# Optimization experiments

Measured on AMD Instinct MI355X. Metric: run time of the kernel, lower is better.

## Reference

```python
import jax, jax.numpy as jnp
import numpy as np

B, IN, H, OUT = 1_000_000, 64, 128, 2


def setup_inputs() -> dict:
    key = jax.random.key(0)
    k1, k2, k3, k4 = jax.random.split(key, 4)
    x = jax.random.normal(k1, (B, IN), dtype=jnp.float32)
    u = jax.random.randint(k2, (B,), 0, 3, dtype=jnp.int64)
    # Xavier-uniform-ish init for weights, zeros for biases (as in the module)
    lim1 = float(np.sqrt(6.0 / (IN + H)))
    W1 = jax.random.uniform(k3, (H, IN), dtype=jnp.float32, minval=-lim1, maxval=lim1)
    b1 = jnp.zeros((H,), dtype=jnp.float32)
    lim2 = float(np.sqrt(6.0 / (H + OUT)))
    Wb = jax.random.uniform(k4, (3, OUT, H), dtype=jnp.float32, minval=-lim2, maxval=lim2)
    bb = jnp.zeros((3, OUT), dtype=jnp.float32)
    return {"x": x, "u": u, "W1": W1, "b1": b1, "Wb": Wb, "bb": bb}


def reference(x, u, W1, b1, Wb, bb):
    # shared trunk: linear + relu  -> [B, H]
    h = jax.nn.relu(x @ W1.T + b1)
    # compute all 3 branch heads in one batched GEMM -> [B, 3, OUT]
    out_all = jnp.einsum("bh,koh->bko", h, Wb) + bb
    # hard routing: select head k = u[b] per row (equivalent to gather->scatter)
    u_idx = u.reshape(-1).astype(jnp.int32)
    out = jnp.take_along_axis(out_all, u_idx[:, None, None], axis=1)[:, 0, :]
    return out
```

## Files before the change

### kernel.cpp

```cpp
#include <hip/hip_runtime.h>
#include <stdint.h>


typedef float f32x4 __attribute__((ext_vector_type(4)));
typedef int   i32x4 __attribute__((ext_vector_type(4)));
typedef short short8 __attribute__((ext_vector_type(8)));
typedef __bf16 bf16x8 __attribute__((ext_vector_type(8)));

#define GLOBAL_AS __attribute__((address_space(1)))
#define LDS_AS    __attribute__((address_space(3)))

static __device__ __forceinline__ f32x4 mfma16(bf16x8 a, bf16x8 b, f32x4 c) {
    return __builtin_amdgcn_mfma_f32_16x16x32_bf16(a, b, c, 0, 0, 0);
}

__global__ __launch_bounds__(256) void coil_fused(
    const float* __restrict__ x,
    const int*   __restrict__ u,
    const float* __restrict__ W1,
    const float* __restrict__ b1,
    const float* __restrict__ Wb,
    const float* __restrict__ bb,
    float* __restrict__ out,
    int nPairs, int nWaves)
{
    __shared__ short w1s[128 * 64];
    __shared__ float b1s[128];
    __shared__ float xsl[4][2048];

    const int tid  = threadIdx.x;
    const int lane = tid & 63;
    const int c    = lane & 15;
    const int g    = lane >> 4;
    const int wsl  = tid >> 6;

    for (int qq = tid; qq < 1024; qq += 256) {
        int row = qq >> 3;
        const float* src = W1 + row * 64 + (qq & 7) * 8;
        short8 v;
        #pragma unroll
        for (int j = 0; j < 8; ++j) v[j] = __builtin_bit_cast(short, (__bf16)src[j]);
        int phys = (qq * 16) ^ ((row & 7) << 4);
        *reinterpret_cast<short8*>(reinterpret_cast<char*>(w1s) + phys) = v;
    }
    if (tid < 128) b1s[tid] = b1[tid];

    const int ko = c;
    const bool kvalid = (ko < 6);
    bf16x8 B2[4];
    #pragma unroll
    for (int s = 0; s < 4; ++s) {
        #pragma unroll
        for (int j = 0; j < 8; ++j) {
            int n = 32 * s + ((j >> 2) << 4) + 4 * g + (j & 3);
            B2[s][j] = kvalid ? (__bf16)Wb[ko * 128 + n] : (__bf16)0.0f;
        }
    }
    const float bbr = kvalid ? bb[ko] : 0.0f;
    const int khead = ko >> 1, opos = ko & 1;

    __syncthreads();

    int xoff[8];
    #pragma unroll
    for (int i = 0; i < 8; ++i) {
        int p = i * 1024 + lane * 16;
        xoff[i] = p ^ (((p >> 8) & 7) << 4);
    }

    const int sw  = (c & 7) << 4;
    const int r00 = (c * 256 + g * 32 +   0) ^ sw;
    const int r01 = (c * 256 + g * 32 +  16) ^ sw;
    const int r10 = (c * 256 + g * 32 + 128) ^ sw;
    const int r11 = (c * 256 + g * 32 + 144) ^ sw;

    const char* xb8 = reinterpret_cast<const char*>(x);
    const char* w1b = reinterpret_cast<const char*>(w1s);
    float* slot = &xsl[wsl][0];
    LDS_AS char* dst = (LDS_AS char*)slot;
    const char* sb = reinterpret_cast<const char*>(slot);

    auto stage = [&](int pairIdx, i32x4& uvA, i32x4& uvB) {
        const int t0 = pairIdx * 2;
        uvA = *reinterpret_cast<const i32x4*>(u + t0 * 16 + 4 * g);
        uvB = *reinterpret_cast<const i32x4*>(u + t0 * 16 + 16 + 4 * g);
        const char* src = xb8 + (size_t)t0 * 4096;
        #pragma unroll
        for (int i = 0; i < 8; ++i)
            __builtin_amdgcn_global_load_lds((const GLOBAL_AS void*)(src + xoff[i]),
                                             (LDS_AS void*)(dst + i * 1024), 16, 0, 0);
    };

    const int w = blockIdx.x * 4 + wsl;
    const int qv = nPairs / nWaves, rm = nPairs % nWaves;
    int p          = w * qv + (w < rm ? w : rm);
    const int pend = p + qv + (w < rm ? 1 : 0);
    if (p >= pend) return;

    i32x4 uvA, uvB, nuvA, nuvB;
    stage(p, uvA, uvB);

    for (; p < pend; ++p) {
        f32x4 xaA = *reinterpret_cast<const f32x4*>(sb + r00);
        f32x4 xbA = *reinterpret_cast<const f32x4*>(sb + r01);
        f32x4 xcA = *reinterpret_cast<const f32x4*>(sb + r10);
        f32x4 xdA = *reinterpret_cast<const f32x4*>(sb + r11);
        f32x4 xaB = *reinterpret_cast<const f32x4*>(sb + 4096 + r00);
        f32x4 xbB = *reinterpret_cast<const f32x4*>(sb + 4096 + r01);
        f32x4 xcB = *reinterpret_cast<const f32x4*>(sb + 4096 + r10);
        f32x4 xdB = *reinterpret_cast<const f32x4*>(sb + 4096 + r11);

        asm volatile("s_waitcnt lgkmcnt(0)" ::: "memory");

        stage((p + 1 < pend) ? p + 1 : p, nuvA, nuvB);

        bf16x8 B1aA, B1bA, B1aB, B1bB;
        #pragma unroll
        for (int j = 0; j < 4; ++j) {
            B1aA[j] = (__bf16)xaA[j];  B1aA[4 + j] = (__bf16)xbA[j];
            B1bA[j] = (__bf16)xcA[j];  B1bA[4 + j] = (__bf16)xdA[j];
            B1aB[j] = (__bf16)xaB[j];  B1aB[4 + j] = (__bf16)xbB[j];
            B1bB[j] = (__bf16)xcB[j];  B1bB[4 + j] = (__bf16)xdB[j];
        }

        f32x4 oaccA = {0.f, 0.f, 0.f, 0.f};
        f32x4 oaccB = {0.f, 0.f, 0.f, 0.f};
        #pragma unroll
        for (int s = 0; s < 4; ++s) {
            const int t0 = 2 * s, t1 = 2 * s + 1;
            f32x4 bia0 = *reinterpret_cast<const f32x4*>(&b1s[16 * t0 + 4 * g]);
            f32x4 bia1 = *reinterpret_cast<const f32x4*>(&b1s[16 * t1 + 4 * g]);
            const int lo0 = (16 * t0 + c) * 128 + 16 * g;
            const int lo1 = (16 * t1 + c) * 128 + 16 * g;
            short8 A00 = *reinterpret_cast<const short8*>(w1b + (lo0 ^ sw));
            short8 A01 = *reinterpret_cast<const short8*>(w1b + ((lo0 + 64) ^ sw));
            short8 A10 = *reinterpret_cast<const short8*>(w1b + (lo1 ^ sw));
            short8 A11 = *reinterpret_cast<const short8*>(w1b + ((lo1 + 64) ^ sw));
            f32x4 h0A = bia0, h1A = bia1, h0B = bia0, h1B = bia1;
            h0A = mfma16(__builtin_bit_cast(bf16x8, A00), B1aA, h0A);
            h0B = mfma16(__builtin_bit_cast(bf16x8, A00), B1aB, h0B);
            h1A = mfma16(__builtin_bit_cast(bf16x8, A10), B1aA, h1A);
            h1B = mfma16(__builtin_bit_cast(bf16x8, A10), B1aB, h1B);
            h0A = mfma16(__builtin_bit_cast(bf16x8, A01), B1bA, h0A);
            h0B = mfma16(__builtin_bit_cast(bf16x8, A01), B1bB, h0B);
            h1A = mfma16(__builtin_bit_cast(bf16x8, A11), B1bA, h1A);
            h1B = mfma16(__builtin_bit_cast(bf16x8, A11), B1bB, h1B);
            bf16x8 A2A, A2B;
            #pragma unroll
            for (int j = 0; j < 4; ++j) {
                A2A[j]     = (__bf16)fmaxf(h0A[j], 0.0f);
                A2A[4 + j] = (__bf16)fmaxf(h1A[j], 0.0f);
                A2B[j]     = (__bf16)fmaxf(h0B[j], 0.0f);
                A2B[4 + j] = (__bf16)fmaxf(h1B[j], 0.0f);
            }
            oaccA = mfma16(A2A, B2[s], oaccA);
            oaccB = mfma16(A2B, B2[s], oaccB);
        }

        const int m0 = p * 32 + 4 * g;
        if (khead == uvA[0]) out[(m0 +  0) * 2 + opos] = oaccA[0] + bbr;
        if (khead == uvA[1]) out[(m0 +  1) * 2 + opos] = oaccA[1] + bbr;
        if (khead == uvA[2]) out[(m0 +  2) * 2 + opos] = oaccA[2] + bbr;
        if (khead == uvA[3]) out[(m0 +  3) * 2 + opos] = oaccA[3] + bbr;
        if (khead == uvB[0]) out[(m0 + 16) * 2 + opos] = oaccB[0] + bbr;
        if (khead == uvB[1]) out[(m0 + 17) * 2 + opos] = oaccB[1] + bbr;
        if (khead == uvB[2]) out[(m0 + 18) * 2 + opos] = oaccB[2] + bbr;
        if (khead == uvB[3]) out[(m0 + 19) * 2 + opos] = oaccB[3] + bbr;

        uvA = nuvA; uvB = nuvB;
    }
}

extern "C" void kernel_launch(void* const* d_in, const int* in_sizes, int n_in,
                              void* d_out, int out_size, void* d_ws, size_t ws_size,
                              hipStream_t stream) {
    const float* x  = (const float*)d_in[0];
    const int*   u  = (const int*)d_in[1];
    const float* W1 = (const float*)d_in[2];
    const float* b1 = (const float*)d_in[3];
    const float* Wb = (const float*)d_in[4];
    const float* bb = (const float*)d_in[5];
    float* out = (float*)d_out;

    const int B = in_sizes[1];
    const int nTiles = B / 16;
    const int nPairs = nTiles / 2;

    int blocks = 768;
    int nWaves = blocks * 4;
    if (nWaves > nPairs) { blocks = (nPairs + 3) / 4; nWaves = blocks * 4; }

    hipLaunchKernelGGL(coil_fused, dim3(blocks), dim3(256), 0, stream,
                       x, u, W1, b1, Wb, bb, out, nPairs, nWaves);
}
```

Measured before the change: 53.17 us.

## Hold W1 fragments in registers and shrink blocks to two waves

The W1 tile is no longer staged into LDS; each lane now loads its bf16 A-fragments straight into 16 register vectors, which removes the per-iteration LDS reads of W1. Blocks shrink to 128 threads with 1536 blocks, and the prologue is reordered so the first x prefetch is issued before the W1 load. The MFMA chains for the two row tiles are serialised to limit live accumulators. In exchange, register pressure per wave rises (64 extra VGPRs for W1) and may lower occupancy, while less LDS is needed per block.

```diff
diff --git a/kernel.cpp b/kernel.cpp
--- a/kernel.cpp
+++ b/kernel.cpp
@@ -14,7 +14,7 @@
     return __builtin_amdgcn_mfma_f32_16x16x32_bf16(a, b, c, 0, 0, 0);
 }
 
-__global__ __launch_bounds__(256) void coil_fused(
+__global__ __launch_bounds__(128) void coil_fused(
     const float* __restrict__ x,
     const int*   __restrict__ u,
     const float* __restrict__ W1,
@@ -24,9 +24,8 @@
     float* __restrict__ out,
     int nPairs, int nWaves)
 {
-    __shared__ short w1s[128 * 64];
     __shared__ float b1s[128];
-    __shared__ float xsl[4][2048];
+    __shared__ float xsl[2][2048];
 
     const int tid  = threadIdx.x;
     const int lane = tid & 63;
@@ -34,16 +33,55 @@
     const int g    = lane >> 4;
     const int wsl  = tid >> 6;
 
-    for (int qq = tid; qq < 1024; qq += 256) {
-        int row = qq >> 3;
-        const float* src = W1 + row * 64 + (qq & 7) * 8;
-        short8 v;
-        #pragma unroll
-        for (int j = 0; j < 8; ++j) v[j] = __builtin_bit_cast(short, (__bf16)src[j]);
-        int phys = (qq * 16) ^ ((row & 7) << 4);
-        *reinterpret_cast<short8*>(reinterpret_cast<char*>(w1s) + phys) = v;
-    }
-    if (tid < 128) b1s[tid] = b1[tid];
+    int xoff[8];
+    #pragma unroll
+    for (int i = 0; i < 8; ++i) {
+        int pb = i * 1024 + lane * 16;
+        xoff[i] = pb ^ (((pb >> 8) & 7) << 4);
+    }
+
+    const char* xb8 = reinterpret_cast<const char*>(x);
+    float* slot = &xsl[wsl][0];
+    LDS_AS char* dst = (LDS_AS char*)slot;
+    const char* sb = reinterpret_cast<const char*>(slot);
+
+    auto stage = [&](int pairIdx, i32x4& uvA, i32x4& uvB) {
+        const int t0 = pairIdx * 2;
+        uvA = *reinterpret_cast<const i32x4*>(u + t0 * 16 + 4 * g);
+        uvB = *reinterpret_cast<const i32x4*>(u + t0 * 16 + 16 + 4 * g);
+        const char* src = xb8 + (size_t)t0 * 4096;
+        #pragma unroll
+        for (int i = 0; i < 8; ++i)
+            __builtin_amdgcn_global_load_lds((const GLOBAL_AS void*)(src + xoff[i]),
+                                             (LDS_AS void*)(dst + i * 1024), 16, 0, 0);
+    };
+
+    const int w = blockIdx.x * 2 + wsl;
+    const int qv = nPairs / nWaves, rm = nPairs % nWaves;
+    int p          = w * qv + (w < rm ? w : rm);
+    const int pend = p + qv + (w < rm ? 1 : 0);
+
+    i32x4 uvA, uvB, nuvA, nuvB;
+    if (p < pend) stage(p, uvA, uvB);
+
+    bf16x8 A0[8], A1[8];
+    {
+        const float* wr = W1 + c * 64 + 8 * g;
+        #pragma unroll
+        for (int t = 0; t < 8; ++t) {
+            f32x4 p0 = *reinterpret_cast<const f32x4*>(wr + t * 1024);
+            f32x4 p1 = *reinterpret_cast<const f32x4*>(wr + t * 1024 + 4);
+            f32x4 p2 = *reinterpret_cast<const f32x4*>(wr + t * 1024 + 32);
+            f32x4 p3 = *reinterpret_cast<const f32x4*>(wr + t * 1024 + 36);
+            #pragma unroll
+            for (int j = 0; j < 4; ++j) {
+                A0[t][j]     = (__bf16)p0[j];
+                A0[t][4 + j] = (__bf16)p1[j];
+                A1[t][j]     = (__bf16)p2[j];
+                A1[t][4 + j] = (__bf16)p3[j];
+            }
+        }
+    }
 
     const int ko = c;
     const bool kvalid = (ko < 6);
@@ -59,46 +97,16 @@
     const float bbr = kvalid ? bb[ko] : 0.0f;
     const int khead = ko >> 1, opos = ko & 1;
 
+    b1s[tid] = b1[tid];
     __syncthreads();
 
-    int xoff[8];
-    #pragma unroll
-    for (int i = 0; i < 8; ++i) {
-        int p = i * 1024 + lane * 16;
-        xoff[i] = p ^ (((p >> 8) & 7) << 4);
-    }
+    if (p >= pend) return;
 
     const int sw  = (c & 7) << 4;
     const int r00 = (c * 256 + g * 32 +   0) ^ sw;
     const int r01 = (c * 256 + g * 32 +  16) ^ sw;
     const int r10 = (c * 256 + g * 32 + 128) ^ sw;
     const int r11 = (c * 256 + g * 32 + 144) ^ sw;
-
-    const char* xb8 = reinterpret_cast<const char*>(x);
-    const char* w1b = reinterpret_cast<const char*>(w1s);
-    float* slot = &xsl[wsl][0];
-    LDS_AS char* dst = (LDS_AS char*)slot;
-    const char* sb = reinterpret_cast<const char*>(slot);
-
-    auto stage = [&](int pairIdx, i32x4& uvA, i32x4& uvB) {
-        const int t0 = pairIdx * 2;
-        uvA = *reinterpret_cast<const i32x4*>(u + t0 * 16 + 4 * g);
-        uvB = *reinterpret_cast<const i32x4*>(u + t0 * 16 + 16 + 4 * g);
-        const char* src = xb8 + (size_t)t0 * 4096;
-        #pragma unroll
-        for (int i = 0; i < 8; ++i)
-            __builtin_amdgcn_global_load_lds((const GLOBAL_AS void*)(src + xoff[i]),
-                                             (LDS_AS void*)(dst + i * 1024), 16, 0, 0);
-    };
-
-    const int w = blockIdx.x * 4 + wsl;
-    const int qv = nPairs / nWaves, rm = nPairs % nWaves;
-    int p          = w * qv + (w < rm ? w : rm);
-    const int pend = p + qv + (w < rm ? 1 : 0);
-    if (p >= pend) return;
-
-    i32x4 uvA, uvB, nuvA, nuvB;
-    stage(p, uvA, uvB);
 
     for (; p < pend; ++p) {
         f32x4 xaA = *reinterpret_cast<const f32x4*>(sb + r00);
@@ -112,7 +120,7 @@
 
         asm volatile("s_waitcnt lgkmcnt(0)" ::: "memory");
 
-        stage((p + 1 < pend) ? p + 1 : p, nuvA, nuvB);
+        if (p + 1 < pend) stage(p + 1, nuvA, nuvB);
 
         bf16x8 B1aA, B1bA, B1aB, B1bB;
         #pragma unroll
@@ -130,31 +138,29 @@
             const int t0 = 2 * s, t1 = 2 * s + 1;
             f32x4 bia0 = *reinterpret_cast<const f32x4*>(&b1s[16 * t0 + 4 * g]);
             f32x4 bia1 = *reinterpret_cast<const f32x4*>(&b1s[16 * t1 + 4 * g]);
-            const int lo0 = (16 * t0 + c) * 128 + 16 * g;
-            const int lo1 = (16 * t1 + c) * 128 + 16 * g;
-            short8 A00 = *reinterpret_cast<const short8*>(w1b + (lo0 ^ sw));
-            short8 A01 = *reinterpret_cast<const short8*>(w1b + ((lo0 + 64) ^ sw));
-            short8 A10 = *reinterpret_cast<const short8*>(w1b + (lo1 ^ sw));
-            short8 A11 = *reinterpret_cast<const short8*>(w1b + ((lo1 + 64) ^ sw));
-            f32x4 h0A = bia0, h1A = bia1, h0B = bia0, h1B = bia1;
-            h0A = mfma16(__builtin_bit_cast(bf16x8, A00), B1aA, h0A);
-            h0B = mfma16(__builtin_bit_cast(bf16x8, A00), B1aB, h0B);
-            h1A = mfma16(__builtin_bit_cast(bf16x8, A10), B1aA, h1A);
-            h1B = mfma16(__builtin_bit_cast(bf16x8, A10), B1aB, h1B);
-            h0A = mfma16(__builtin_bit_cast(bf16x8, A01), B1bA, h0A);
-            h0B = mfma16(__builtin_bit_cast(bf16x8, A01), B1bB, h0B);
-            h1A = mfma16(__builtin_bit_cast(bf16x8, A11), B1bA, h1A);
-            h1B = mfma16(__builtin_bit_cast(bf16x8, A11), B1bB, h1B);
-            bf16x8 A2A, A2B;
+            f32x4 h0 = bia0, h1 = bia1;
+            h0 = mfma16(A0[t0], B1aA, h0);
+            h1 = mfma16(A0[t1], B1aA, h1);
+            h0 = mfma16(A1[t0], B1bA, h0);
+            h1 = mfma16(A1[t1], B1bA, h1);
+            bf16x8 A2;
             #pragma unroll
             for (int j = 0; j < 4; ++j) {
-                A2A[j]     = (__bf16)fmaxf(h0A[j], 0.0f);
-                A2A[4 + j] = (__bf16)fmaxf(h1A[j], 0.0f);
-                A2B[j]     = (__bf16)fmaxf(h0B[j], 0.0f);
-                A2B[4 + j] = (__bf16)fmaxf(h1B[j], 0.0f);
+                A2[j]     = (__bf16)fmaxf(h0[j], 0.0f);
+                A2[4 + j] = (__bf16)fmaxf(h1[j], 0.0f);
             }
-            oaccA = mfma16(A2A, B2[s], oaccA);
-            oaccB = mfma16(A2B, B2[s], oaccB);
+            oaccA = mfma16(A2, B2[s], oaccA);
+            h0 = bia0; h1 = bia1;
+            h0 = mfma16(A0[t0], B1aB, h0);
+            h1 = mfma16(A0[t1], B1aB, h1);
+            h0 = mfma16(A1[t0], B1bB, h0);
+            h1 = mfma16(A1[t1], B1bB, h1);
+            #pragma unroll
+            for (int j = 0; j < 4; ++j) {
+                A2[j]     = (__bf16)fmaxf(h0[j], 0.0f);
+                A2[4 + j] = (__bf16)fmaxf(h1[j], 0.0f);
+            }
+            oaccB = mfma16(A2, B2[s], oaccB);
         }
 
         const int m0 = p * 32 + 4 * g;
@@ -186,10 +192,10 @@
     const int nTiles = B / 16;
     const int nPairs = nTiles / 2;
 
-    int blocks = 768;
-    int nWaves = blocks * 4;
-    if (nWaves > nPairs) { blocks = (nPairs + 3) / 4; nWaves = blocks * 4; }
-
-    hipLaunchKernelGGL(coil_fused, dim3(blocks), dim3(256), 0, stream,
+    int blocks = 1536;
+    int nWaves = blocks * 2;
+    if (nWaves > nPairs) { blocks = (nPairs + 1) / 2; nWaves = blocks * 2; }
+
+    hipLaunchKernelGGL(coil_fused, dim3(blocks), dim3(128), 0, stream,
                        x, u, W1, b1, Wb, bb, out, nPairs, nWaves);
 }
```

Measured after the change: 68.82 us. 1.29x slower.
